# Kernel tuning notes

Hardware: AMD Instinct MI355X
Metric: run time of the kernel (lower is better)

Reference implementation:

```python
import jax, jax.numpy as jnp
import numpy as np

B, T = 64, 32
F_DIM, V = 1024, 4000
H = V  # hidden_size == vocab_size in the module


def setup_inputs() -> dict:
    key = jax.random.key(0)
    ks = jax.random.split(key, 10)
    s = 1.0 / np.sqrt(H)  # torch LSTM init: U(-1/sqrt(H), 1/sqrt(H))
    u = lambda k, shp: jax.random.uniform(k, shp, jnp.float32, -s, s)
    return {
        "features": jax.random.normal(ks[0], (B, F_DIM), jnp.float32),
        "captions": jax.random.randint(ks[1], (B, T), 0, V, jnp.int32),
        "W_ih0": u(ks[2], (4 * H, F_DIM + V)),
        "W_hh0": u(ks[3], (4 * H, H)),
        "b_ih0": u(ks[4], (4 * H,)),
        "b_hh0": u(ks[5], (4 * H,)),
        "W_ih1": u(ks[6], (4 * H, H)),
        "W_hh1": u(ks[7], (4 * H, H)),
        "b_ih1": u(ks[8], (4 * H,)),
        "b_hh1": u(ks[9], (4 * H,)),
    }


def _lstm_cell(pre, h, c, W_hh, b_hh):
    # pre: precomputed input-to-hidden contribution [B, 4H]
    g = pre + h @ W_hh.T + b_hh
    i, f, gg, o = jnp.split(g, 4, axis=-1)  # torch gate order i,f,g,o
    c = jax.nn.sigmoid(f) * c + jax.nn.sigmoid(i) * jnp.tanh(gg)
    h = jax.nn.sigmoid(o) * jnp.tanh(c)
    return h, c


def reference(features, W_ih0, W_hh0, b_ih0, b_hh0, W_ih1, W_hh1, b_ih1, b_hh1, captions):
    Bb, Tt = captions.shape
    dt = features.dtype
    # Input at step t (t=1..T-1) is concat(features, onehot(captions[:, t-1])).
    # onehot @ W_v.T is a row-gather of W_v.T -> no dense onehot materialized.
    W_f = W_ih0[:, :F_DIM]            # [4H, F]
    W_v = W_ih0[:, F_DIM:]            # [4H, V]
    feat_pre = features @ W_f.T       # [B, 4H], time-invariant
    tok_pre = W_v.T[captions[:, : Tt - 1]]  # [B, T-1, 4H]
    ih0 = feat_pre[:, None, :] + tok_pre + b_ih0
    xs = jnp.swapaxes(ih0, 0, 1)      # [T-1, B, 4H]

    init = tuple(jnp.zeros((Bb, H), dt) for _ in range(4))

    def step(carry, pre0):
        h0, c0, h1, c1 = carry
        h0, c0 = _lstm_cell(pre0, h0, c0, W_hh0, b_hh0)
        pre1 = h0 @ W_ih1.T + b_ih1
        h1, c1 = _lstm_cell(pre1, h1, c1, W_hh1, b_hh1)
        return (h0, c0, h1, c1), h1

    _, ys = jax.lax.scan(step, init, xs)  # [T-1, B, H]
    # outputs[:, 0, :] stays zeros in the original (loop starts at t=1)
    outs = jnp.concatenate([jnp.zeros((Bb, 1, H), dt), jnp.swapaxes(ys, 0, 1)], axis=1)
    return outs
```

## Files before the change

kernel.cpp:

```cpp
#include <hip/hip_runtime.h>

#define DEVINL __device__ __forceinline__

typedef __attribute__((ext_vector_type(4))) float f32x4;
typedef __attribute__((ext_vector_type(8))) short s16x8;
typedef __attribute__((ext_vector_type(4))) unsigned short u16x4;
typedef __attribute__((ext_vector_type(8))) unsigned short u16x8;

static constexpr int HDIM = 4000;
static constexpr int G4   = 16000;
static constexpr int FD   = 1024;
static constexpr int LD0  = 5024;
static constexpr int TT   = 31;
static constexpr int NJ   = 64 * 31;
static constexpr int KCT  = 125;

DEVINL float bf2f(unsigned short u) {
  unsigned v = (unsigned)u << 16;
  return __builtin_bit_cast(float, v);
}
DEVINL unsigned short f2bf(float x) {
  unsigned u = __builtin_bit_cast(unsigned, x);
  u += 0x7fffu + ((u >> 16) & 1u);
  return (unsigned short)(u >> 16);
}
DEVINL float sigm(float x) { return 1.f / (1.f + __expf(-x)); }
DEVINL float tanh_(float x) { float e = __expf(2.f * x); return (e - 1.f) / (e + 1.f); }

#define MFMA_BF16 __builtin_amdgcn_mfma_f32_16x16x32_bf16

DEVINL void mfma8(s16x8 a0, s16x8 a1, const unsigned short* __restrict__ bp,
                  f32x4 acc[2][4]) {
  s16x8 b0 = *(const s16x8*)(bp);
  s16x8 b1 = *(const s16x8*)(bp + 128);
  s16x8 b2 = *(const s16x8*)(bp + 256);
  s16x8 b3 = *(const s16x8*)(bp + 384);
  acc[0][0] = MFMA_BF16(a0, b0, acc[0][0], 0, 0, 0);
  acc[0][1] = MFMA_BF16(a0, b1, acc[0][1], 0, 0, 0);
  acc[0][2] = MFMA_BF16(a0, b2, acc[0][2], 0, 0, 0);
  acc[0][3] = MFMA_BF16(a0, b3, acc[0][3], 0, 0, 0);
  acc[1][0] = MFMA_BF16(a1, b0, acc[1][0], 0, 0, 0);
  acc[1][1] = MFMA_BF16(a1, b1, acc[1][1], 0, 0, 0);
  acc[1][2] = MFMA_BF16(a1, b2, acc[1][2], 0, 0, 0);
  acc[1][3] = MFMA_BF16(a1, b3, acc[1][3], 0, 0, 0);
}

DEVINL void gpair(const unsigned short* __restrict__ W0,
                  const unsigned short* __restrict__ W1,
                  const unsigned short* __restrict__ hP,
                  int kc0, int kc1, int dir, int lane, int lr, int lg,
                  f32x4 acc[2][4]) {
  int n = kc1 - kc0;
  #pragma unroll 2
  for (int s = 0; s < n; ++s) {
    int kc = dir ? (kc1 - 1 - s) : (kc0 + s);
    s16x8 a0 = *(const s16x8*)(W0 + (size_t)kc * 512 + lane * 8);
    s16x8 a1 = *(const s16x8*)(W1 + (size_t)kc * 512 + lane * 8);
    mfma8(a0, a1, hP + (size_t)kc * 2048 + (lg * 64 + lr) * 8, acc);
  }
}

template <bool HH>
DEVINL void gpair2(const unsigned short* __restrict__ Wi0,
                   const unsigned short* __restrict__ Wi1,
                   const unsigned short* __restrict__ Wh0,
                   const unsigned short* __restrict__ Wh1,
                   const unsigned short* __restrict__ h0P,
                   const unsigned short* __restrict__ h1P,
                   int kc0, int kc1, int dir, int lane, int lr, int lg,
                   f32x4 acc[2][4]) {
  int n = kc1 - kc0;
  #pragma unroll 1
  for (int s = 0; s < n; ++s) {
    int kc = dir ? (kc1 - 1 - s) : (kc0 + s);
    size_t woff = (size_t)kc * 512 + lane * 8;
    size_t boff = (size_t)kc * 2048 + (lg * 64 + lr) * 8;
    s16x8 ai0 = *(const s16x8*)(Wi0 + woff);
    s16x8 ai1 = *(const s16x8*)(Wi1 + woff);
    mfma8(ai0, ai1, h0P + boff, acc);
    if (HH) {
      s16x8 ah0 = *(const s16x8*)(Wh0 + woff);
      s16x8 ah1 = *(const s16x8*)(Wh1 + woff);
      mfma8(ah0, ah1, h1P + boff, acc);
    }
  }
}

DEVINL void reduce_acc(float gl[2][4][16][64], f32x4 acc[2][4],
                       int gp, int kq, int lr, int lg) {
  for (int rnd = 0; rnd < 4; ++rnd) {
    if ((kq >> 1) == rnd) {
      int slot = kq & 1;
      #pragma unroll
      for (int j = 0; j < 2; ++j) {
        int g = 2 * gp + j;
        #pragma unroll
        for (int n0 = 0; n0 < 4; ++n0)
          #pragma unroll
          for (int e = 0; e < 4; ++e) {
            float* d = &gl[slot][g][4 * lg + e][(n0 << 4) + lr];
            if (rnd == 0) *d = acc[j][n0][e];
            else          *d += acc[j][n0][e];
          }
      }
    }
    __syncthreads();
  }
}

__global__ void to_bf16_k(const float* __restrict__ s, unsigned short* __restrict__ d, long n) {
  long i = (((long)blockIdx.x * blockDim.x) + threadIdx.x) * 8;
  if (i >= n) return;
  f32x4 a = *(const f32x4*)(s + i);
  f32x4 b = *(const f32x4*)(s + i + 4);
  u16x8 o;
  o[0] = f2bf(a[0]); o[1] = f2bf(a[1]); o[2] = f2bf(a[2]); o[3] = f2bf(a[3]);
  o[4] = f2bf(b[0]); o[5] = f2bf(b[1]); o[6] = f2bf(b[2]); o[7] = f2bf(b[3]);
  *(u16x8*)(d + i) = o;
}

__global__ __launch_bounds__(256) void pack_k(const float* __restrict__ W,
                                              unsigned short* __restrict__ P) {
  int wv = (blockIdx.x << 2) + (threadIdx.x >> 6);
  int lane = threadIdx.x & 63, lr = lane & 15, lg = lane >> 4;
  int rb = wv / 500; int rem = wv - rb * 500;
  int g = rem / KCT; int kc = rem - g * KCT;
  int row = g * 4000 + rb * 16 + lr;
  int col = kc * 32 + lg * 8;
  const float* sp = W + (size_t)row * 4000 + col;
  f32x4 a = *(const f32x4*)sp;
  f32x4 b = *(const f32x4*)(sp + 4);
  u16x8 o;
  o[0] = f2bf(a[0]); o[1] = f2bf(a[1]); o[2] = f2bf(a[2]); o[3] = f2bf(a[3]);
  o[4] = f2bf(b[0]); o[5] = f2bf(b[1]); o[6] = f2bf(b[2]); o[7] = f2bf(b[3]);
  *(u16x8*)(P + ((size_t)wv * 64 + lane) * 8) = o;
}

__global__ void wf_conv_k(const float* __restrict__ s, unsigned short* __restrict__ d) {
  int idx = blockIdx.x * blockDim.x + threadIdx.x;
  int r = idx >> 7;
  int k8 = (idx & 127) << 3;
  const float* sp = s + (size_t)r * LD0 + k8;
  f32x4 a = *(const f32x4*)sp;
  f32x4 b = *(const f32x4*)(sp + 4);
  u16x8 o;
  o[0] = f2bf(a[0]); o[1] = f2bf(a[1]); o[2] = f2bf(a[2]); o[3] = f2bf(a[3]);
  o[4] = f2bf(b[0]); o[5] = f2bf(b[1]); o[6] = f2bf(b[2]); o[7] = f2bf(b[3]);
  *(u16x8*)(d + (size_t)r * FD + k8) = o;
}

DEVINL void gemm16u(const unsigned short* __restrict__ W,
                    const unsigned short* __restrict__ Hb,
                    int K, int kbeg, int kend, int lr, int lg, f32x4* acc) {
  const unsigned short* wp  = W  + (size_t)lr * K + 8 * lg + kbeg;
  const unsigned short* hp0 = Hb + (size_t)lr * K + 8 * lg + kbeg;
  const unsigned short* hp1 = hp0 + (size_t)16 * K;
  const unsigned short* hp2 = hp0 + (size_t)32 * K;
  const unsigned short* hp3 = hp0 + (size_t)48 * K;
  int nk = kend - kbeg;
  #pragma unroll 2
  for (int k = 0; k < nk; k += 32) {
    s16x8 a  = *(const s16x8*)(wp  + k);
    s16x8 b0 = *(const s16x8*)(hp0 + k);
    s16x8 b1 = *(const s16x8*)(hp1 + k);
    s16x8 b2 = *(const s16x8*)(hp2 + k);
    s16x8 b3 = *(const s16x8*)(hp3 + k);
    acc[0] = MFMA_BF16(a, b0, acc[0], 0, 0, 0);
    acc[1] = MFMA_BF16(a, b1, acc[1], 0, 0, 0);
    acc[2] = MFMA_BF16(a, b2, acc[2], 0, 0, 0);
    acc[3] = MFMA_BF16(a, b3, acc[3], 0, 0, 0);
  }
}

__global__ __launch_bounds__(512, 2) void featpre_k(
    const unsigned short* __restrict__ Wf, const unsigned short* __restrict__ Fb,
    const float* __restrict__ bih0, float* __restrict__ fp0) {
  __shared__ float gl[2][4][16][64];
  int tid = threadIdx.x, lane = tid & 63, wid = tid >> 6;
  int lr = lane & 15, lg = lane >> 4;
  int sub = wid & 3, kh = wid >> 2;
  int rowblk = blockIdx.x << 6;
  size_t row0 = (size_t)rowblk + (sub << 4);
  f32x4 acc[4] = {};
  gemm16u(Wf + row0 * FD, Fb, FD, kh ? 512 : 0, kh ? 1024 : 512, lr, lg, acc);
  #pragma unroll
  for (int n0 = 0; n0 < 4; ++n0)
    #pragma unroll
    for (int e = 0; e < 4; ++e)
      gl[kh][sub][4 * lg + e][(n0 << 4) + lr] = acc[n0][e];
  __syncthreads();
  for (int n = tid; n < 4096; n += 512) {
    int i = n & 63, b = n >> 6;
    int r = rowblk + i;
    float v = gl[0][i >> 4][i & 15][b] + gl[1][i >> 4][i & 15][b] + bih0[r];
    fp0[(size_t)b * G4 + r] = v;
  }
}

__global__ __launch_bounds__(256) void gather_k(
    const float* __restrict__ Wih0, const int* __restrict__ caps,
    const float* __restrict__ fp0, unsigned short* __restrict__ ih0T) {
  __shared__ unsigned short wv[4][4000];
  int r0 = blockIdx.x << 2;
  for (int rr = 0; rr < 4; ++rr) {
    const float* src = Wih0 + (size_t)(r0 + rr) * LD0 + FD;
    for (int c4 = threadIdx.x; c4 < 1000; c4 += 256) {
      f32x4 v = *(const f32x4*)(src + c4 * 4);
      u16x4 o;
      o[0] = f2bf(v[0]); o[1] = f2bf(v[1]); o[2] = f2bf(v[2]); o[3] = f2bf(v[3]);
      *(u16x4*)(&wv[rr][c4 * 4]) = o;
    }
  }
  __syncthreads();
  for (int j = threadIdx.x; j < NJ; j += 256) {
    int b = j / TT, t = j - b * TT;
    int tok = caps[(b << 5) + t];
    f32x4 f = *(const f32x4*)(fp0 + (size_t)b * G4 + r0);
    #pragma unroll
    for (int rr = 0; rr < 4; ++rr)
      ih0T[(size_t)(r0 + rr) * NJ + j] = f2bf(f[rr] + bf2f(wv[rr][tok]));
  }
}

__global__ __launch_bounds__(256) void tj_k(const unsigned short* __restrict__ src,
                                            unsigned short* __restrict__ dst) {
  __shared__ unsigned short tile[32][34];
  int r0 = blockIdx.x << 5;
  int j0 = blockIdx.y << 5;
  int c = threadIdx.x & 31, q = threadIdx.x >> 5;
  #pragma unroll
  for (int e = 0; e < 4; ++e) {
    int rr = q + e * 8;
    tile[rr][c] = src[(size_t)(r0 + rr) * NJ + j0 + c];
  }
  __syncthreads();
  #pragma unroll
  for (int e = 0; e < 4; ++e) {
    int jj = q + e * 8;
    dst[(size_t)(j0 + jj) * G4 + r0 + c] = tile[c][jj];
  }
}

DEVINL size_t hpk(int r, int b) {
  return ((size_t)(r >> 3) * 64 + b) * 8 + (r & 7);
}

__global__ __launch_bounds__(1024, 1) void fused_step_k(
    const unsigned short* __restrict__ pWhh0, const unsigned short* __restrict__ pWih1,
    const unsigned short* __restrict__ pWhh1,
    unsigned short* __restrict__ h0b, unsigned short* __restrict__ h1b,
    float* __restrict__ c0, float* __restrict__ c1,
    const unsigned short* __restrict__ ih0J,
    const float* __restrict__ bhh0, const float* __restrict__ bih1,
    const float* __restrict__ bhh1, float* __restrict__ out, int p) {
  __shared__ float gl[2][4][16][64];
  int tid = threadIdx.x, lane = tid & 63, wid = tid >> 6;
  int lr = lane & 15, lg = lane >> 4;
  int gp = wid & 1, kq = wid >> 1;
  int kc0 = (kq * KCT) >> 3, kc1 = ((kq + 1) * KCT) >> 3;
  int dir = p & 1;
  int i = tid & 15, bb = tid >> 4;
  int r = (blockIdx.x << 4) + i;
  size_t ci = (size_t)bb * HDIM + r;
  size_t wo0 = ((size_t)(blockIdx.x * 4 + 2 * gp) * KCT) * 512;
  size_t wo1 = wo0 + (size_t)KCT * 512;

  for (int half = 0; half < 2; ++half) {
    bool run_l0 = (half == dir);
    if (run_l0) {
      if (p >= TT) continue;
      const unsigned short* h0_in = h0b + (size_t)((p ^ 1) & 1) * 256000;
      unsigned short* h0_out      = h0b + (size_t)(p & 1) * 256000;
      f32x4 acc[2][4] = {};
      if (p > 0)
        gpair(pWhh0 + wo0, pWhh0 + wo1, h0_in, kc0, kc1, dir, lane, lr, lg, acc);
      reduce_acc(gl, acc, gp, kq, lr, lg);
      const unsigned short* ih = ih0J + (size_t)(bb * TT + p) * G4;
      float gi = gl[0][0][i][bb] + gl[1][0][i][bb] + bf2f(ih[r])            + bhh0[r];
      float gf = gl[0][1][i][bb] + gl[1][1][i][bb] + bf2f(ih[HDIM + r])     + bhh0[HDIM + r];
      float gg = gl[0][2][i][bb] + gl[1][2][i][bb] + bf2f(ih[2 * HDIM + r]) + bhh0[2 * HDIM + r];
      float go = gl[0][3][i][bb] + gl[1][3][i][bb] + bf2f(ih[3 * HDIM + r]) + bhh0[3 * HDIM + r];
      float cn = sigm(gf) * c0[ci] + sigm(gi) * tanh_(gg);
      float hn = sigm(go) * tanh_(cn);
      c0[ci] = cn;
      h0_out[hpk(r, bb)] = f2bf(hn);
      __syncthreads();
    } else {
      if (p < 1) continue;
      int t = p - 1;
      const unsigned short* h0_t  = h0b + (size_t)(t & 1) * 256000;
      const unsigned short* h1_in = h1b + (size_t)((t ^ 1) & 1) * 256000;
      unsigned short* h1_out      = h1b + (size_t)(t & 1) * 256000;
      f32x4 acc[2][4] = {};
      if (t > 0)
        gpair2<true>(pWih1 + wo0, pWih1 + wo1, pWhh1 + wo0, pWhh1 + wo1,
                     h0_t, h1_in, kc0, kc1, dir, lane, lr, lg, acc);
      else
        gpair2<false>(pWih1 + wo0, pWih1 + wo1, pWhh1 + wo0, pWhh1 + wo1,
                      h0_t, h1_in, kc0, kc1, dir, lane, lr, lg, acc);
      reduce_acc(gl, acc, gp, kq, lr, lg);
      float gi = gl[0][0][i][bb] + gl[1][0][i][bb] + bih1[r]            + bhh1[r];
      float gf = gl[0][1][i][bb] + gl[1][1][i][bb] + bih1[HDIM + r]     + bhh1[HDIM + r];
      float gg = gl[0][2][i][bb] + gl[1][2][i][bb] + bih1[2 * HDIM + r] + bhh1[2 * HDIM + r];
      float go = gl[0][3][i][bb] + gl[1][3][i][bb] + bih1[3 * HDIM + r] + bhh1[3 * HDIM + r];
      float cn = sigm(gf) * c1[ci] + sigm(gi) * tanh_(gg);
      float hn = sigm(go) * tanh_(cn);
      c1[ci] = cn;
      h1_out[hpk(r, bb)] = f2bf(hn);
      out[(size_t)bb * (32 * HDIM) + (size_t)(t + 1) * HDIM + r] = hn;
      __syncthreads();
    }
  }
}

__global__ void sentinel_k(float* o) { o[0] = -123456.f; }

extern "C" void kernel_launch(void* const* d_in, const int* in_sizes, int n_in,
                              void* d_out, int out_size, void* d_ws, size_t ws_size,
                              hipStream_t stream) {
  (void)in_sizes; (void)n_in;
  const float* features = (const float*)d_in[0];
  const int*   captions = (const int*)d_in[1];
  const float* W_ih0    = (const float*)d_in[2];
  const float* W_hh0    = (const float*)d_in[3];
  const float* b_ih0    = (const float*)d_in[4];
  const float* b_hh0    = (const float*)d_in[5];
  const float* W_ih1    = (const float*)d_in[6];
  const float* W_hh1    = (const float*)d_in[7];
  const float* b_ih1    = (const float*)d_in[8];
  const float* b_hh1    = (const float*)d_in[9];
  float* out = (float*)d_out;

  char* w = (char*)d_ws;
  unsigned short* h0b   = (unsigned short*)(w);
  unsigned short* h1b   = (unsigned short*)(w + 1024000);
  float*          c0    = (float*)(w + 2048000);
  float*          c1    = (float*)(w + 3072000);
  unsigned short* pWhh0 = (unsigned short*)(w + 4096000);
  unsigned short* pWih1 = (unsigned short*)(w + 132096000);
  unsigned short* pWhh1 = (unsigned short*)(w + 260096000);
  unsigned short* bWf   = (unsigned short*)(w + 388096000);
  unsigned short* ih0T  = (unsigned short*)(w + 420864000);
  float*          fp0   = (float*)(w + 484352000);
  unsigned short* bFeat = (unsigned short*)(w + 488448000);
  unsigned short* ih0J  = (unsigned short*)(w + 488579328);
  const size_t NEED = 552067328;
  if (ws_size < NEED) { sentinel_k<<<1, 1, 0, stream>>>(out); return; }

  hipMemsetAsync(d_out, 0, (size_t)out_size * 4, stream);
  hipMemsetAsync(w, 0, 4096000, stream);

  pack_k<<<31250, 256, 0, stream>>>(W_hh0, pWhh0);
  pack_k<<<31250, 256, 0, stream>>>(W_ih1, pWih1);
  pack_k<<<31250, 256, 0, stream>>>(W_hh1, pWhh1);
  to_bf16_k<<<32,    256, 0, stream>>>(features, bFeat, 65536L);
  wf_conv_k<<<8000,  256, 0, stream>>>(W_ih0, bWf);
  featpre_k<<<250,   512, 0, stream>>>(bWf, bFeat, b_ih0, fp0);
  gather_k<<<4000,   256, 0, stream>>>(W_ih0, captions, fp0, ih0T);
  tj_k<<<dim3(500, 62), 256, 0, stream>>>(ih0T, ih0J);

  for (int p = 0; p <= TT; ++p) {
    fused_step_k<<<250, 1024, 0, stream>>>(pWhh0, pWih1, pWhh1, h0b, h1b, c0, c1,
                                           ih0J, b_hh0, b_ih1, b_hh1, out, p);
  }
}
```

Before: 2.865 ms.

## Replace per-step kernel launches with persistent kernel using grid barrier

The 32 per-timestep launches become one persistent kernel of 250 blocks that loops over timesteps and synchronises with a custom atomic grid barrier (arrive flags gathered by block 0, then a go flag). The cell states c0/c1 now stay in registers, and the biases are loaded once instead of going through global memory every step. This removes launch overhead and the per-step state traffic. It relies on all 250 blocks being co-resident (one 1024-thread block per CU) and on the barrier being correct, otherwise it can deadlock.

```diff
diff --git a/kernel.cpp b/kernel.cpp
--- a/kernel.cpp
+++ b/kernel.cpp
@@ -14,6 +14,7 @@
 static constexpr int TT   = 31;
 static constexpr int NJ   = 64 * 31;
 static constexpr int KCT  = 125;
+static constexpr unsigned NBLK = 250;
 
 DEVINL float bf2f(unsigned short u) {
   unsigned v = (unsigned)u << 16;
@@ -245,71 +246,109 @@
   return ((size_t)(r >> 3) * 64 + b) * 8 + (r & 7);
 }
 
-__global__ __launch_bounds__(1024, 1) void fused_step_k(
+DEVINL void gridbar2(unsigned* __restrict__ arrive, unsigned* __restrict__ go,
+                     unsigned val) {
+  __syncthreads();
+  if (threadIdx.x == 0) {
+    __threadfence();
+    __hip_atomic_store(&arrive[blockIdx.x * 32], val, __ATOMIC_RELEASE,
+                       __HIP_MEMORY_SCOPE_AGENT);
+  }
+  if (blockIdx.x == 0) {
+    if (threadIdx.x < NBLK) {
+      while (__hip_atomic_load(&arrive[threadIdx.x * 32], __ATOMIC_ACQUIRE,
+                               __HIP_MEMORY_SCOPE_AGENT) < val) {}
+    }
+    __syncthreads();
+    if (threadIdx.x == 0)
+      __hip_atomic_store(go, val, __ATOMIC_RELEASE, __HIP_MEMORY_SCOPE_AGENT);
+  }
+  if (threadIdx.x == 0) {
+    while (__hip_atomic_load(go, __ATOMIC_ACQUIRE,
+                             __HIP_MEMORY_SCOPE_AGENT) < val) {
+      __builtin_amdgcn_s_sleep(1);
+    }
+  }
+  __syncthreads();
+  __threadfence();
+}
+
+__global__ __launch_bounds__(1024, 1) void lstm_persist2_k(
     const unsigned short* __restrict__ pWhh0, const unsigned short* __restrict__ pWih1,
     const unsigned short* __restrict__ pWhh1,
     unsigned short* __restrict__ h0b, unsigned short* __restrict__ h1b,
-    float* __restrict__ c0, float* __restrict__ c1,
     const unsigned short* __restrict__ ih0J,
     const float* __restrict__ bhh0, const float* __restrict__ bih1,
-    const float* __restrict__ bhh1, float* __restrict__ out, int p) {
+    const float* __restrict__ bhh1, float* __restrict__ out,
+    unsigned* __restrict__ bar) {
   __shared__ float gl[2][4][16][64];
   int tid = threadIdx.x, lane = tid & 63, wid = tid >> 6;
   int lr = lane & 15, lg = lane >> 4;
   int gp = wid & 1, kq = wid >> 1;
   int kc0 = (kq * KCT) >> 3, kc1 = ((kq + 1) * KCT) >> 3;
-  int dir = p & 1;
   int i = tid & 15, bb = tid >> 4;
   int r = (blockIdx.x << 4) + i;
-  size_t ci = (size_t)bb * HDIM + r;
   size_t wo0 = ((size_t)(blockIdx.x * 4 + 2 * gp) * KCT) * 512;
   size_t wo1 = wo0 + (size_t)KCT * 512;
-
-  for (int half = 0; half < 2; ++half) {
-    bool run_l0 = (half == dir);
-    if (run_l0) {
-      if (p >= TT) continue;
-      const unsigned short* h0_in = h0b + (size_t)((p ^ 1) & 1) * 256000;
-      unsigned short* h0_out      = h0b + (size_t)(p & 1) * 256000;
-      f32x4 acc[2][4] = {};
-      if (p > 0)
-        gpair(pWhh0 + wo0, pWhh0 + wo1, h0_in, kc0, kc1, dir, lane, lr, lg, acc);
-      reduce_acc(gl, acc, gp, kq, lr, lg);
-      const unsigned short* ih = ih0J + (size_t)(bb * TT + p) * G4;
-      float gi = gl[0][0][i][bb] + gl[1][0][i][bb] + bf2f(ih[r])            + bhh0[r];
-      float gf = gl[0][1][i][bb] + gl[1][1][i][bb] + bf2f(ih[HDIM + r])     + bhh0[HDIM + r];
-      float gg = gl[0][2][i][bb] + gl[1][2][i][bb] + bf2f(ih[2 * HDIM + r]) + bhh0[2 * HDIM + r];
-      float go = gl[0][3][i][bb] + gl[1][3][i][bb] + bf2f(ih[3 * HDIM + r]) + bhh0[3 * HDIM + r];
-      float cn = sigm(gf) * c0[ci] + sigm(gi) * tanh_(gg);
-      float hn = sigm(go) * tanh_(cn);
-      c0[ci] = cn;
-      h0_out[hpk(r, bb)] = f2bf(hn);
-      __syncthreads();
-    } else {
-      if (p < 1) continue;
-      int t = p - 1;
-      const unsigned short* h0_t  = h0b + (size_t)(t & 1) * 256000;
-      const unsigned short* h1_in = h1b + (size_t)((t ^ 1) & 1) * 256000;
-      unsigned short* h1_out      = h1b + (size_t)(t & 1) * 256000;
-      f32x4 acc[2][4] = {};
-      if (t > 0)
-        gpair2<true>(pWih1 + wo0, pWih1 + wo1, pWhh1 + wo0, pWhh1 + wo1,
-                     h0_t, h1_in, kc0, kc1, dir, lane, lr, lg, acc);
-      else
-        gpair2<false>(pWih1 + wo0, pWih1 + wo1, pWhh1 + wo0, pWhh1 + wo1,
-                      h0_t, h1_in, kc0, kc1, dir, lane, lr, lg, acc);
-      reduce_acc(gl, acc, gp, kq, lr, lg);
-      float gi = gl[0][0][i][bb] + gl[1][0][i][bb] + bih1[r]            + bhh1[r];
-      float gf = gl[0][1][i][bb] + gl[1][1][i][bb] + bih1[HDIM + r]     + bhh1[HDIM + r];
-      float gg = gl[0][2][i][bb] + gl[1][2][i][bb] + bih1[2 * HDIM + r] + bhh1[2 * HDIM + r];
-      float go = gl[0][3][i][bb] + gl[1][3][i][bb] + bih1[3 * HDIM + r] + bhh1[3 * HDIM + r];
-      float cn = sigm(gf) * c1[ci] + sigm(gi) * tanh_(gg);
-      float hn = sigm(go) * tanh_(cn);
-      c1[ci] = cn;
-      h1_out[hpk(r, bb)] = f2bf(hn);
-      out[(size_t)bb * (32 * HDIM) + (size_t)(t + 1) * HDIM + r] = hn;
-      __syncthreads();
-    }
+  unsigned* arrive = bar;
+  unsigned* go = bar + 8192;
+
+  float bh0[4], bi1[4], bh1[4];
+  #pragma unroll
+  for (int g = 0; g < 4; ++g) {
+    bh0[g] = bhh0[g * HDIM + r];
+    bi1[g] = bih1[g * HDIM + r];
+    bh1[g] = bhh1[g * HDIM + r];
+  }
+  float c0r = 0.f, c1r = 0.f;
+
+  for (int p = 0; p <= TT; ++p) {
+    int dir = p & 1;
+    for (int half = 0; half < 2; ++half) {
+      bool run_l0 = (half == dir);
+      if (run_l0) {
+        if (p >= TT) continue;
+        const unsigned short* h0_in = h0b + (size_t)((p ^ 1) & 1) * 256000;
+        unsigned short* h0_out      = h0b + (size_t)(p & 1) * 256000;
+        f32x4 acc[2][4] = {};
+        if (p > 0)
+          gpair(pWhh0 + wo0, pWhh0 + wo1, h0_in, kc0, kc1, dir, lane, lr, lg, acc);
+        reduce_acc(gl, acc, gp, kq, lr, lg);
+        const unsigned short* ih = ih0J + (size_t)(bb * TT + p) * G4;
+        float gi = gl[0][0][i][bb] + gl[1][0][i][bb] + bf2f(ih[r])            + bh0[0];
+        float gf = gl[0][1][i][bb] + gl[1][1][i][bb] + bf2f(ih[HDIM + r])     + bh0[1];
+        float gg = gl[0][2][i][bb] + gl[1][2][i][bb] + bf2f(ih[2 * HDIM + r]) + bh0[2];
+        float go_ = gl[0][3][i][bb] + gl[1][3][i][bb] + bf2f(ih[3 * HDIM + r]) + bh0[3];
+        c0r = sigm(gf) * c0r + sigm(gi) * tanh_(gg);
+        float hn = sigm(go_) * tanh_(c0r);
+        h0_out[hpk(r, bb)] = f2bf(hn);
+        __syncthreads();
+      } else {
+        if (p < 1) continue;
+        int t = p - 1;
+        const unsigned short* h0_t  = h0b + (size_t)(t & 1) * 256000;
+        const unsigned short* h1_in = h1b + (size_t)((t ^ 1) & 1) * 256000;
+        unsigned short* h1_out      = h1b + (size_t)(t & 1) * 256000;
+        f32x4 acc[2][4] = {};
+        if (t > 0)
+          gpair2<true>(pWih1 + wo0, pWih1 + wo1, pWhh1 + wo0, pWhh1 + wo1,
+                       h0_t, h1_in, kc0, kc1, dir, lane, lr, lg, acc);
+        else
+          gpair2<false>(pWih1 + wo0, pWih1 + wo1, pWhh1 + wo0, pWhh1 + wo1,
+                        h0_t, h1_in, kc0, kc1, dir, lane, lr, lg, acc);
+        reduce_acc(gl, acc, gp, kq, lr, lg);
+        float gi = gl[0][0][i][bb] + gl[1][0][i][bb] + bi1[0] + bh1[0];
+        float gf = gl[0][1][i][bb] + gl[1][1][i][bb] + bi1[1] + bh1[1];
+        float gg = gl[0][2][i][bb] + gl[1][2][i][bb] + bi1[2] + bh1[2];
+        float go_ = gl[0][3][i][bb] + gl[1][3][i][bb] + bi1[3] + bh1[3];
+        c1r = sigm(gf) * c1r + sigm(gi) * tanh_(gg);
+        float hn = sigm(go_) * tanh_(c1r);
+        h1_out[hpk(r, bb)] = f2bf(hn);
+        out[(size_t)bb * (32 * HDIM) + (size_t)(t + 1) * HDIM + r] = hn;
+        __syncthreads();
+      }
+    }
+    if (p < TT) gridbar2(arrive, go, (unsigned)(p + 1));
   }
 }
 
@@ -334,8 +373,6 @@
   char* w = (char*)d_ws;
   unsigned short* h0b   = (unsigned short*)(w);
   unsigned short* h1b   = (unsigned short*)(w + 1024000);
-  float*          c0    = (float*)(w + 2048000);
-  float*          c1    = (float*)(w + 3072000);
   unsigned short* pWhh0 = (unsigned short*)(w + 4096000);
   unsigned short* pWih1 = (unsigned short*)(w + 132096000);
   unsigned short* pWhh1 = (unsigned short*)(w + 260096000);
@@ -344,11 +381,12 @@
   float*          fp0   = (float*)(w + 484352000);
   unsigned short* bFeat = (unsigned short*)(w + 488448000);
   unsigned short* ih0J  = (unsigned short*)(w + 488579328);
-  const size_t NEED = 552067328;
+  unsigned*       bar   = (unsigned*)(w + 552067328);
+  const size_t NEED = 552104192;
   if (ws_size < NEED) { sentinel_k<<<1, 1, 0, stream>>>(out); return; }
 
   hipMemsetAsync(d_out, 0, (size_t)out_size * 4, stream);
-  hipMemsetAsync(w, 0, 4096000, stream);
+  hipMemsetAsync(w + 552067328, 0, 36864, stream);
 
   pack_k<<<31250, 256, 0, stream>>>(W_hh0, pWhh0);
   pack_k<<<31250, 256, 0, stream>>>(W_ih1, pWih1);
@@ -359,8 +397,6 @@
   gather_k<<<4000,   256, 0, stream>>>(W_ih0, captions, fp0, ih0T);
   tj_k<<<dim3(500, 62), 256, 0, stream>>>(ih0T, ih0J);
 
-  for (int p = 0; p <= TT; ++p) {
-    fused_step_k<<<250, 1024, 0, stream>>>(pWhh0, pWih1, pWhh1, h0b, h1b, c0, c1,
-                                           ih0J, b_hh0, b_ih1, b_hh1, out, p);
-  }
-}
+  lstm_persist2_k<<<NBLK, 1024, 0, stream>>>(pWhh0, pWih1, pWhh1, h0b, h1b,
+                                             ih0J, b_hh0, b_ih1, b_hh1, out, bar);
+}
```

Result: slower. 5.604 ms (+95.6%).
